# Kernel tuning notes

Measured on AMD Instinct MI355X. Metric: run time of the kernel, lower is better.

## Reference

```python
import jax, jax.numpy as jnp
import numpy as np
import math

B, S, D = 2, 2048, 1024
LKV, LQ = 512, 768
H, HD = 16, 64          # decop_rot_dim must equal head_dim (code reshapes rot proj to head_dim)
E, NS, K = 8, 2, 2      # routed experts, shared experts, top-k
EPS = 1e-6


def rmsnorm(x, w):
    xf = x.astype(jnp.float32)
    n = xf * jax.lax.rsqrt(jnp.mean(xf * xf, axis=-1, keepdims=True) + EPS)
    return w * n.astype(x.dtype)


def rope(x, cos, sin):
    # x: (B,S,H,HD); cos/sin: (S, HD//2). Pairs are consecutive elements (view_as_complex).
    xr = x.reshape(*x.shape[:-1], HD // 2, 2)
    x0, x1 = xr[..., 0], xr[..., 1]
    c = cos[None, :, None, :]
    s = sin[None, :, None, :]
    o0 = x0 * c - x1 * s
    o1 = x0 * s + x1 * c
    return jnp.stack([o0, o1], axis=-1).reshape(x.shape)


def _expert(x, W1, b1, W2, b2):
    # Expert: Linear -> ReLU -> Linear -> Dropout(0.5); dropout is identity at eval.
    return jax.nn.relu(x @ W1 + b1) @ W2 + b2


def setup_inputs() -> dict:
    key = jax.random.key(0)
    ks = jax.random.split(key, 20)
    g = lambda i, shape: jax.random.normal(ks[i], shape, jnp.float32) * 0.02
    inv_freq = 1.0 / (10000.0 ** (jnp.arange(0, HD, 2, dtype=jnp.float32) / HD))
    ang = jnp.arange(S, dtype=jnp.float32)[:, None] * inv_freq[None, :]  # (S, HD//2)
    return {
        'x': jax.random.normal(ks[0], (B, S, D), jnp.float32),
        'freqs_cos': jnp.cos(ang),
        'freqs_sin': jnp.sin(ang),
        'router_noise': jax.random.normal(ks[1], (B, S, E), jnp.float32),
        'rms1_w': jnp.ones((D,), jnp.float32),
        'rms2_w': jnp.ones((D,), jnp.float32),
        'w_lq': g(2, (D, LQ)), 'w_lkv': g(3, (D, LKV)),
        'w_q': g(4, (LQ, H * HD)), 'w_k': g(5, (LKV, H * HD)), 'w_v': g(6, (LKV, H * HD)),
        'w_qr': g(7, (LQ, H * HD)), 'b_qr': jnp.zeros((H * HD,), jnp.float32),
        'w_kr': g(8, (D, H * HD)), 'b_kr': jnp.zeros((H * HD,), jnp.float32),
        'w_o': g(9, (H * HD, D)), 'b_o': jnp.zeros((D,), jnp.float32),
        'w_route': g(10, (D, E)), 'b_route': jnp.zeros((E,), jnp.float32),
        'w_noise': g(11, (D, E)), 'b_noise': jnp.zeros((E,), jnp.float32),
        'rW1': g(12, (E, D, 4 * D)), 'rb1': jnp.zeros((E, 4 * D), jnp.float32),
        'rW2': g(13, (E, 4 * D, D)), 'rb2': jnp.zeros((E, D), jnp.float32),
        'sW1': g(14, (NS, D, 4 * D)), 'sb1': jnp.zeros((NS, 4 * D), jnp.float32),
        'sW2': g(15, (NS, 4 * D, D)), 'sb2': jnp.zeros((NS, D), jnp.float32),
    }


def _forward(x, freqs_cos, freqs_sin, router_noise, rms1_w, rms2_w,
             w_lq, w_lkv, w_q, w_k, w_v, w_qr, b_qr, w_kr, b_kr, w_o, b_o,
             w_route, b_route, w_noise, b_noise,
             rW1, rb1, rW2, rb2, sW1, sb1, sW2, sb2):
    Bq, Sq, Dq = x.shape
    # --- MLA attention branch ---
    h = rmsnorm(x, rms1_w)
    cq = h @ w_lq          # (B,S,LQ)
    ckv = h @ w_lkv        # (B,S,LKV)
    q = (cq @ w_q).reshape(Bq, Sq, H, HD)
    qr = rope((cq @ w_qr + b_qr).reshape(Bq, Sq, H, HD), freqs_cos, freqs_sin)
    k = (ckv @ w_k).reshape(Bq, Sq, H, HD)
    kr = rope((h @ w_kr + b_kr).reshape(Bq, Sq, H, HD), freqs_cos, freqs_sin)
    v = (ckv @ w_v).reshape(Bq, Sq, H, HD)
    qf = jnp.concatenate([q, qr], axis=-1)  # (B,S,H,2*HD)
    kf = jnp.concatenate([k, kr], axis=-1)
    scores = jnp.einsum('bqhd,bkhd->bhqk', qf, kf) / math.sqrt(HD)  # scale by sqrt(head_dim), as in source
    att = jax.nn.softmax(scores.astype(jnp.float32), axis=-1).astype(qf.dtype)
    attn_out = jnp.einsum('bhqk,bkhd->bqhd', att, v).reshape(Bq, Sq, H * HD)
    x = x + attn_out @ w_o + b_o
    # --- DeepSeek MoE branch ---
    h2 = rmsnorm(x, rms2_w)
    r_act = h2 @ w_route + b_route
    noisy = r_act + router_noise * jax.nn.softplus(h2 @ w_noise + b_noise)
    topv, idx = jax.lax.top_k(noisy, K)
    # softmax over -inf-filled sparse logits == softmax over top-k values scattered to idx
    wk = jax.nn.softmax(topv, axis=-1)  # (B,S,K)
    gate = jnp.einsum('btk,btke->bte', wk, jax.nn.one_hot(idx, E, dtype=h2.dtype))  # zeros off top-k
    f = jnp.zeros_like(h2)
    for i in range(E):  # fixed small expert loop; gate is exactly 0 for unrouted tokens
        f = f + gate[..., i:i + 1] * _expert(h2, rW1[i], rb1[i], rW2[i], rb2[i])
    for j in range(NS):
        f = f + _expert(h2, sW1[j], sb1[j], sW2[j], sb2[j])
    # DeepSeekMoE returns x_in + f_out where x_in = rmsnorm output; Block adds residual
    return x + h2 + f


def reference(x, freqs_cos, freqs_sin, router_noise, rms1_w, rms2_w,
              w_lq, w_lkv, w_q, w_k, w_v, w_qr, b_qr, w_kr, b_kr, w_o, b_o,
              w_route, b_route, w_noise, b_noise,
              rW1, rb1, rW2, rb2, sW1, sb1, sW2, sb2):
    return _forward(x, freqs_cos, freqs_sin, router_noise, rms1_w, rms2_w,
                    w_lq, w_lkv, w_q, w_k, w_v, w_qr, b_qr, w_kr, b_kr, w_o, b_o,
                    w_route, b_route, w_noise, b_noise,
                    rW1, rb1, rW2, rb2, sW1, sb1, sW2, sb2)
```

## Files before the change

### kernel.cpp

```cpp
#include <hip/hip_runtime.h>
#include <cstdint>

typedef unsigned short u16;
typedef unsigned int   u32;
typedef unsigned long long u64;
using short8 = __attribute__((ext_vector_type(8))) short;
using f32x4  = __attribute__((ext_vector_type(4))) float;

#define S_   2048
#define D_   1024
#define NTOK 4096

__device__ __forceinline__ u16 f2bf(float f){
  u32 u = __float_as_uint(f);
  u32 r = u + 0x7fffu + ((u >> 16) & 1u);
  return (u16)(r >> 16);
}
__device__ __forceinline__ float bf2f(u16 h){
  return __uint_as_float(((u32)h) << 16);
}
__device__ __forceinline__ void gld16(const void* g, void* l){
  __builtin_amdgcn_global_load_lds((__attribute__((address_space(1))) void*)(void*)g,
                                   (__attribute__((address_space(3))) void*)l, 16, 0, 0);
}

enum { F_OUTBF16=1, F_BIAS=2, F_RELU=4, F_RESID=8, F_GATEACC=16,
       F_GATHER=64, F_SCATTER=128, F_EXPB=512, F_SPLITK2=1024 };

template<int FLAGS>
__global__ void __launch_bounds__(256, 4)
gemm_k(const u16* __restrict__ A, int lda, long sAz,
       const u16* __restrict__ Bt, int ldb, long sBz,
       void* __restrict__ out, int ldo, long sOz,
       float* __restrict__ out2,
       const float* __restrict__ bias,
       const float* __restrict__ resid,
       const float* __restrict__ gv,
       const int* __restrict__ idx,
       const int* __restrict__ slotb,
       const int* __restrict__ cntp, int ebase,
       int K, int ncols)
{
  constexpr int BM = 128, BK = 32;
  const int tid = threadIdx.x;
  const int w = tid >> 6, l = tid & 63;
  const int wr = w >> 1, wc = w & 1;

  const int gx = gridDim.x, gy = gridDim.y;
  const int nwg = gx*gy*gridDim.z;
  const int flat = (blockIdx.z*gy + blockIdx.y)*gx + blockIdx.x;
  const int q8 = nwg >> 3, r8 = nwg & 7, xcd = flat & 7, off8 = flat >> 3;
  const int swz = (xcd < r8) ? (xcd*(q8+1) + off8)
                             : (r8*(q8+1) + (xcd-r8)*q8 + off8);
  const int tn = swz % gx;
  const int rest = swz / gx;
  const int tm = rest % gy;
  const int z  = rest / gy;
  const int ncol0 = tn * 128;

  int kh = 0, ze = z;
  if constexpr (FLAGS & F_SPLITK2){ kh = z & 1; ze = z >> 1; }

  int cnt = 0x7fffffff; long ofs = 0;
  if constexpr (FLAGS & (F_GATHER|F_SCATTER)){
    const int e = ebase + ze;
    cnt = cntp[e]; ofs = (long)cntp[8+e];
    if (tm*BM >= cnt) return;
  }

  const u16 *Abase, *Btbase;
  if constexpr (FLAGS & F_GATHER){
    Abase  = A;
    Btbase = Bt + (long)ze*sBz + (long)ncol0*ldb;
  } else if constexpr (FLAGS & F_SCATTER){
    Abase  = A + ofs*lda + (long)tm*BM*lda + (long)kh*K;
    Btbase = Bt + (long)ze*sBz + (long)ncol0*ldb + (long)kh*K;
  } else {
    Abase  = A  + (long)ze*sAz + (long)tm*BM*lda + (long)kh*K;
    Btbase = Bt + (long)ze*sBz + (long)ncol0*ldb + (long)kh*K;
  }

  const int r0 = tid >> 2, seg = tid & 3;
  long aoff0, aoff1;
  if constexpr (FLAGS & F_GATHER){
    const int p0 = tm*BM + r0, p1 = p0 + 64;
    const int t0 = (p0 < cnt) ? idx[ofs + p0] : 0;
    const int t1 = (p1 < cnt) ? idx[ofs + p1] : 0;
    aoff0 = (long)t0*lda; aoff1 = (long)t1*lda;
  } else {
    aoff0 = (long)r0*lda; aoff1 = (long)(r0+64)*lda;
  }
  const u16* pA0 = Abase + aoff0 + seg*8;
  const u16* pA1 = Abase + aoff1 + seg*8;
  const u16* pB0 = Btbase + (long)r0*ldb + seg*8;
  const u16* pB1 = Btbase + (long)(r0+64)*ldb + seg*8;

  __shared__ __align__(16) u16 As[2][BM*BK];
  __shared__ __align__(16) u16 Bs[2][BM*BK];

  f32x4 zero = {0.f,0.f,0.f,0.f};
  f32x4 acc[4][4];
  #pragma unroll
  for (int i=0;i<4;i++)
    #pragma unroll
    for (int j=0;j<4;j++) acc[i][j] = zero;

  const int NK = K >> 5;

  auto stage = [&](int buf, int kt){
    const int k0 = kt*BK;
    gld16(pA0 + k0, &As[buf][(w*64)*8]);
    gld16(pA1 + k0, &As[buf][(256 + w*64)*8]);
    gld16(pB0 + k0, &Bs[buf][(w*64)*8]);
    gld16(pB1 + k0, &Bs[buf][(256 + w*64)*8]);
  };

  stage(0,0);
  __syncthreads();

  for (int kt=0; kt<NK; ++kt){
    const int cur = kt & 1, nxt = cur ^ 1;
    if (kt+1 < NK) stage(nxt, kt+1);
    short8 a[4], b[4];
    #pragma unroll
    for (int m=0;m<4;m++){
      const int arow = wr*64 + m*16 + (l & 15);
      a[m] = *(const short8*)&As[cur][arow*BK + (l>>4)*8];
    }
    #pragma unroll
    for (int n=0;n<4;n++){
      const int brow = wc*64 + n*16 + (l & 15);
      b[n] = *(const short8*)&Bs[cur][brow*BK + (l>>4)*8];
    }
    #pragma unroll
    for (int m=0;m<4;m++)
      #pragma unroll
      for (int n=0;n<4;n++)
        acc[m][n] = __builtin_amdgcn_mfma_f32_16x16x32_bf16(a[m], b[n], acc[m][n], 0, 0, 0);
    __syncthreads();
  }

  float* outf = (float*)out + (long)z*sOz;
  u16*   outh = (u16*)out + (long)z*sOz;
  const float* bp = bias;
  if constexpr (FLAGS & F_EXPB) bp += (long)(ebase+ze)*ncols;
  const long row0 = (long)tm*BM + wr*64;
  #pragma unroll
  for (int m=0;m<4;m++){
    #pragma unroll
    for (int n=0;n<4;n++){
      const int col = ncol0 + wc*64 + n*16 + (l & 15);
      if (col < ncols){
        #pragma unroll
        for (int r=0;r<4;r++){
          const long row = row0 + m*16 + ((l>>4)*4) + r;
          float v = acc[m][n][r];
          if constexpr (FLAGS & F_BIAS){
            bool addb = true;
            if constexpr (FLAGS & F_SPLITK2) addb = (kh == 0);
            if (addb) v += bp[col];
          }
          if constexpr (FLAGS & F_RELU) v = fmaxf(v, 0.f);
          if constexpr (FLAGS & F_SCATTER){
            if (row < cnt){
              const long gs = ofs + row;
              const int tok = idx[gs];
              float* dst = (float*)out + (long)(slotb[gs]*2 + kh)*sOz;
              dst[(long)tok*ldo + col] = gv[gs] * v;
            }
          } else if constexpr (FLAGS & F_GATHER){
            if (row < cnt) outh[(ofs + row)*(long)ldo + col] = f2bf(v);
          } else if constexpr (FLAGS & F_GATEACC){
            outf[row*(long)ldo + col] += v;
          } else if constexpr (FLAGS & F_RESID){
            const long off = row*(long)ldo + col;
            outf[off] = resid[off] + v;
          } else if constexpr (FLAGS & F_OUTBF16){
            outh[row*(long)ldo + col] = f2bf(v);
          } else {
            outf[row*(long)ldo + col] = v;
          }
        }
      }
    }
  }
}

#define LDP 136

__global__ void __launch_bounds__(256, 2)
flash_k(const u16* __restrict__ qf, const u16* __restrict__ kf,
        const u16* __restrict__ vt, u16* __restrict__ attn)
{
  const int bh = blockIdx.x;
  const int qt = blockIdx.y;
  const int b = bh >> 4, h = bh & 15;
  const int tid = threadIdx.x, w = tid >> 6, l = tid & 63;
  const int l4 = l & 15, lh = l >> 4;

  const u16* Qb = qf + (long)b*4194304 + h*128;
  const u16* Kb = kf + (long)b*4194304 + h*128;
  const u16* Vb = vt + (long)bh*131072;
  u16* Ob = attn + (long)b*2097152 + h*64;

  short8 qa[2][4];
  #pragma unroll
  for (int m=0;m<2;m++)
    #pragma unroll
    for (int ks=0;ks<4;ks++){
      const long row = qt*128 + w*32 + m*16 + l4;
      qa[m][ks] = *(const short8*)(Qb + row*2048 + ks*32 + lh*8);
    }

  __shared__ __align__(16) u16 KPs[128*LDP];
  __shared__ __align__(16) u16 Vs[64*LDP];

  const float SCL = 0.125f * 1.44269504f;
  float mst[2][4], lst[2][4];
  f32x4 o_acc[2][4];
  #pragma unroll
  for (int m=0;m<2;m++)
    #pragma unroll
    for (int r=0;r<4;r++){ mst[m][r] = -3.0e38f; lst[m][r] = 0.f; }
  #pragma unroll
  for (int m=0;m<2;m++)
    #pragma unroll
    for (int n=0;n<4;n++) o_acc[m][n] = (f32x4){0.f,0.f,0.f,0.f};

  for (int t=0;t<16;t++){
    #pragma unroll
    for (int i=0;i<8;i++){
      const int c = i*256 + tid;
      const int kr = c >> 4, kc = (c & 15) * 8;
      const uint4 v = *(const uint4*)(Kb + (long)(t*128+kr)*2048 + kc);
      *(uint4*)&KPs[kr*LDP + kc] = v;
    }
    #pragma unroll
    for (int i=0;i<4;i++){
      const int c = i*256 + tid;
      const int vr = c >> 4, vc = (c & 15) * 8;
      const uint4 v = *(const uint4*)(Vb + (long)vr*2048 + t*128 + vc);
      *(uint4*)&Vs[vr*LDP + vc] = v;
    }
    __syncthreads();

    f32x4 s[2][8];
    #pragma unroll
    for (int m=0;m<2;m++)
      #pragma unroll
      for (int n=0;n<8;n++) s[m][n] = (f32x4){0.f,0.f,0.f,0.f};
    #pragma unroll
    for (int ks=0;ks<4;ks++){
      short8 bn[8];
      #pragma unroll
      for (int n=0;n<8;n++)
        bn[n] = *(const short8*)&KPs[(n*16+l4)*LDP + ks*32 + lh*8];
      #pragma unroll
      for (int m=0;m<2;m++)
        #pragma unroll
        for (int n=0;n<8;n++)
          s[m][n] = __builtin_amdgcn_mfma_f32_16x16x32_bf16(qa[m][ks], bn[n], s[m][n], 0,0,0);
    }
    __syncthreads();

    #pragma unroll
    for (int m=0;m<2;m++){
      #pragma unroll
      for (int r=0;r<4;r++){
        float pm = s[m][0][r];
        #pragma unroll
        for (int n=1;n<8;n++) pm = fmaxf(pm, s[m][n][r]);
        #pragma unroll
        for (int o=1;o<16;o<<=1) pm = fmaxf(pm, __shfl_xor(pm, o));
        const float mnew = fmaxf(mst[m][r], pm);
        const float sf = exp2f((mst[m][r] - mnew)*SCL);
        float rsum = 0.f;
        #pragma unroll
        for (int n=0;n<8;n++){
          const float p = exp2f((s[m][n][r] - mnew)*SCL);
          s[m][n][r] = p;
          rsum += p;
        }
        #pragma unroll
        for (int o=1;o<16;o<<=1) rsum += __shfl_xor(rsum, o);
        lst[m][r] = lst[m][r]*sf + rsum;
        mst[m][r] = mnew;
        #pragma unroll
        for (int n=0;n<4;n++) o_acc[m][n][r] *= sf;
      }
    }
    #pragma unroll
    for (int m=0;m<2;m++)
      #pragma unroll
      for (int n=0;n<8;n++)
        #pragma unroll
        for (int r=0;r<4;r++)
          KPs[(w*32 + m*16 + lh*4 + r)*LDP + n*16 + l4] = f2bf(s[m][n][r]);
    __syncthreads();

    #pragma unroll
    for (int ks=0;ks<4;ks++){
      short8 pa[2], vb[4];
      #pragma unroll
      for (int m=0;m<2;m++)
        pa[m] = *(const short8*)&KPs[(w*32 + m*16 + l4)*LDP + ks*32 + lh*8];
      #pragma unroll
      for (int n=0;n<4;n++)
        vb[n] = *(const short8*)&Vs[(n*16+l4)*LDP + ks*32 + lh*8];
      #pragma unroll
      for (int m=0;m<2;m++)
        #pragma unroll
        for (int n=0;n<4;n++)
          o_acc[m][n] = __builtin_amdgcn_mfma_f32_16x16x32_bf16(pa[m], vb[n], o_acc[m][n], 0,0,0);
    }
    __syncthreads();
  }

  #pragma unroll
  for (int m=0;m<2;m++){
    #pragma unroll
    for (int r=0;r<4;r++){
      const long row = qt*128 + w*32 + m*16 + lh*4 + r;
      const float inv = 1.f / lst[m][r];
      #pragma unroll
      for (int n=0;n<4;n++)
        Ob[row*1024 + n*16 + l4] = f2bf(o_acc[m][n][r] * inv);
    }
  }
}

__global__ void tpose_k(const float* __restrict__ src, u16* __restrict__ dst,
                        int K, int N, long szS, long szD)
{
  __shared__ u16 tile[32][36];
  const int t = threadIdx.x;
  src += (long)blockIdx.z*szS; dst += (long)blockIdx.z*szD;
  const int n0 = blockIdx.x*32, k0 = blockIdx.y*32;
  const int lr = t >> 3, lc = (t & 7) * 4;
  const float4 v = *(const float4*)&src[(long)(k0+lr)*N + n0 + lc];
  ushort4 tv; tv.x=f2bf(v.x); tv.y=f2bf(v.y); tv.z=f2bf(v.z); tv.w=f2bf(v.w);
  *(ushort4*)&tile[lr][lc] = tv;
  __syncthreads();
  ushort4 o;
  o.x = tile[lc+0][lr]; o.y = tile[lc+1][lr];
  o.z = tile[lc+2][lr]; o.w = tile[lc+3][lr];
  *(ushort4*)&dst[(long)(n0+lr)*K + k0 + lc] = o;
}

__global__ void vt_k(const u16* __restrict__ src, u16* __restrict__ dst)
{
  __shared__ u16 tile[32][36];
  const int t = threadIdx.x;
  const int z = blockIdx.z;
  const int b = z >> 4, h = z & 15;
  const int s0 = blockIdx.x*32, d0 = blockIdx.y*32;
  const int lr = t >> 3, lc = (t & 7) * 4;
  ushort4 v = *(const ushort4*)&src[(long)(b*2048 + s0+lr)*1024 + h*64 + d0 + lc];
  *(ushort4*)&tile[lr][lc] = v;
  __syncthreads();
  ushort4 o;
  o.x = tile[lc+0][lr]; o.y = tile[lc+1][lr];
  o.z = tile[lc+2][lr]; o.w = tile[lc+3][lr];
  *(ushort4*)&dst[(long)z*131072 + (long)(d0+lr)*2048 + s0 + lc] = o;
}

template<bool WF32>
__global__ void rmsnorm_k(const float* __restrict__ x, const float* __restrict__ w,
                          u16* __restrict__ ob, float* __restrict__ of)
{
  const int row = blockIdx.x, t = threadIdx.x;
  const float4 v = ((const float4*)(x + (long)row*D_))[t];
  float ss = v.x*v.x + v.y*v.y + v.z*v.z + v.w*v.w;
  #pragma unroll
  for (int o=32;o>0;o>>=1) ss += __shfl_down(ss, o);
  __shared__ float red[4];
  if ((t&63)==0) red[t>>6] = ss;
  __syncthreads();
  const float scale = rsqrtf((red[0]+red[1]+red[2]+red[3])*(1.0f/D_) + 1e-6f);
  const float4 wv = ((const float4*)w)[t];
  const float o0=v.x*scale*wv.x, o1=v.y*scale*wv.y, o2=v.z*scale*wv.z, o3=v.w*scale*wv.w;
  const long base = (long)row*D_ + t*4;
  uint2 p; p.x = (u32)f2bf(o0) | ((u32)f2bf(o1)<<16);
  p.y = (u32)f2bf(o2) | ((u32)f2bf(o3)<<16);
  *(uint2*)&ob[base] = p;
  if constexpr (WF32) *(float4*)&of[base] = make_float4(o0,o1,o2,o3);
}

__global__ void rope_concat_k(const u16* __restrict__ qt, const u16* __restrict__ qrt,
                              const u16* __restrict__ kt, const u16* __restrict__ krt,
                              const float* __restrict__ fc, const float* __restrict__ fs,
                              u16* __restrict__ qf, u16* __restrict__ kf)
{
  const int idx = blockIdx.x*256 + threadIdx.x;
  const int j = idx & 31, h = (idx>>5) & 15, bs = idx >> 9;
  if (bs >= NTOK) return;
  const int s = bs & (S_-1);
  const float c = fc[s*32+j], sn = fs[s*32+j];
  const long ib = (long)bs*1024 + h*64 + 2*j;
  const long ob = (long)bs*2048 + h*128 + 2*j;
  *(u32*)&qf[ob] = *(const u32*)&qt[ib];
  *(u32*)&kf[ob] = *(const u32*)&kt[ib];
  float x0 = bf2f(qrt[ib]), x1 = bf2f(qrt[ib+1]);
  *(u32*)&qf[ob+64] = (u32)f2bf(x0*c - x1*sn) | ((u32)f2bf(x0*sn + x1*c) << 16);
  x0 = bf2f(krt[ib]); x1 = bf2f(krt[ib+1]);
  *(u32*)&kf[ob+64] = (u32)f2bf(x0*c - x1*sn) | ((u32)f2bf(x0*sn + x1*c) << 16);
}

__global__ void topk_k(const float* __restrict__ h2, const float* __restrict__ wr,
                       const float* __restrict__ br, const float* __restrict__ wn,
                       const float* __restrict__ bn, const float* __restrict__ noise,
                       int* __restrict__ eids, float2* __restrict__ gates)
{
  const int tok = blockIdx.x, t = threadIdx.x;
  const float4 xv = ((const float4*)(h2 + (long)tok*D_))[t];
  const float xs[4] = {xv.x, xv.y, xv.z, xv.w};
  float ar[8], an[8];
  #pragma unroll
  for (int e=0;e<8;e++){ ar[e]=0.f; an[e]=0.f; }
  #pragma unroll
  for (int i=0;i<4;i++){
    const int d = t*4+i;
    const float* wrr = wr + d*8;
    const float* wnr = wn + d*8;
    #pragma unroll
    for (int e=0;e<8;e++){ ar[e] += xs[i]*wrr[e]; an[e] += xs[i]*wnr[e]; }
  }
  #pragma unroll
  for (int e=0;e<8;e++){
    #pragma unroll
    for (int o=32;o>0;o>>=1){ ar[e] += __shfl_down(ar[e], o); an[e] += __shfl_down(an[e], o); }
  }
  __shared__ float rr[4][8], rn[4][8];
  if ((t&63)==0){
    const int w4 = t>>6;
    #pragma unroll
    for (int e=0;e<8;e++){ rr[w4][e]=ar[e]; rn[w4][e]=an[e]; }
  }
  __syncthreads();
  if (t==0){
    float nz[8];
    #pragma unroll
    for (int e=0;e<8;e++){
      const float r  = rr[0][e]+rr[1][e]+rr[2][e]+rr[3][e] + br[e];
      const float ns = rn[0][e]+rn[1][e]+rn[2][e]+rn[3][e] + bn[e];
      const float sp = (ns > 20.f) ? ns : log1pf(expf(ns));
      nz[e] = r + noise[(long)tok*8+e]*sp;
    }
    int i0 = 0;
    #pragma unroll
    for (int e=1;e<8;e++) if (nz[e] > nz[i0]) i0 = e;
    int i1 = -1; float best = -3.0e38f;
    #pragma unroll
    for (int e=0;e<8;e++) if (e != i0 && nz[e] > best){ best = nz[e]; i1 = e; }
    const float e1  = expf(nz[i1]-nz[i0]);
    const float inv = 1.f/(1.f+e1);
    eids[tok] = i0 | (i1 << 8);
    gates[tok] = make_float2(inv, e1*inv);
  }
}

__global__ void __launch_bounds__(64)
hist_k(const int* __restrict__ eids, int* __restrict__ segcnt)
{
  const int b = blockIdx.x, t = threadIdx.x;
  const int id = eids[b*64 + t];
  const int i0 = id & 255, i1 = (id >> 8) & 255;
  #pragma unroll
  for (int e=0;e<8;e++){
    const u64 m0 = __ballot(i0==e);
    const u64 m1 = __ballot(i1==e);
    if (t==0) segcnt[e*64+b] = __popcll(m0) + __popcll(m1);
  }
}

__global__ void __launch_bounds__(64)
scan_k(const int* __restrict__ segcnt, int* __restrict__ segoff,
       int* __restrict__ cntoff)
{
  const int t = threadIdx.x;
  int base = 0;
  for (int e=0;e<8;e++){
    const int c = segcnt[e*64+t];
    int sc = c;
    #pragma unroll
    for (int o=1;o<64;o<<=1){ int u = __shfl_up(sc, o); if (t >= o) sc += u; }
    const int tot = __shfl(sc, 63);
    segoff[e*64+t] = base + (sc - c);
    if (t==0){ cntoff[e] = tot; cntoff[8+e] = base; }
    base += tot;
  }
}

__global__ void __launch_bounds__(64)
fill_k(const int* __restrict__ eids, const float2* __restrict__ gates,
       const int* __restrict__ segoff, int* __restrict__ idxb,
       float* __restrict__ gvb, int* __restrict__ slotb)
{
  const int b = blockIdx.x, t = threadIdx.x;
  const int tok = b*64 + t;
  const int id = eids[tok];
  const int i0 = id & 255, i1 = (id >> 8) & 255;
  const float2 g = gates[tok];
  const u64 below = ((u64)1 << t) - 1;
  #pragma unroll
  for (int e=0;e<8;e++){
    const u64 m0 = __ballot(i0==e);
    const u64 m1 = __ballot(i1==e);
    if (i0==e){
      const int pos = segoff[e*64+b] + __popcll(m0 & below);
      idxb[pos] = tok; gvb[pos] = g.x; slotb[pos] = 0;
    } else if (i1==e){
      const int pos = segoff[e*64+b] + __popcll(m0) + __popcll(m1 & below);
      idxb[pos] = tok; gvb[pos] = g.y; slotb[pos] = 1;
    }
  }
}

__global__ void addstore_k(const float* __restrict__ a, const float* __restrict__ b,
                           float* __restrict__ o, long n4)
{
  long i = (long)blockIdx.x*blockDim.x + threadIdx.x;
  const long stride = (long)gridDim.x*blockDim.x;
  for (; i<n4; i+=stride){
    const float4 va = ((const float4*)a)[i];
    const float4 vb = ((const float4*)b)[i];
    ((float4*)o)[i] = make_float4(va.x+vb.x, va.y+vb.y, va.z+vb.z, va.w+vb.w);
  }
}
__global__ void addacc4_k(const float* __restrict__ f0, const float* __restrict__ f1,
                          const float* __restrict__ f2, const float* __restrict__ f3,
                          float* __restrict__ o, long n4)
{
  long i = (long)blockIdx.x*blockDim.x + threadIdx.x;
  const long stride = (long)gridDim.x*blockDim.x;
  for (; i<n4; i+=stride){
    const float4 a = ((const float4*)f0)[i];
    const float4 b = ((const float4*)f1)[i];
    const float4 c = ((const float4*)f2)[i];
    const float4 d = ((const float4*)f3)[i];
    float4 vo = ((const float4*)o)[i];
    ((float4*)o)[i] = make_float4(vo.x+a.x+b.x+c.x+d.x, vo.y+a.y+b.y+c.y+d.y,
                                  vo.z+a.z+b.z+c.z+d.z, vo.w+a.w+b.w+c.w+d.w);
  }
}

extern "C" void kernel_launch(void* const* d_in, const int* in_sizes, int n_in,
                              void* d_out, int out_size, void* d_ws, size_t ws_size,
                              hipStream_t stream)
{
  const float* x      = (const float*)d_in[0];
  const float* fcos   = (const float*)d_in[1];
  const float* fsin   = (const float*)d_in[2];
  const float* rnoise = (const float*)d_in[3];
  const float* rms1w  = (const float*)d_in[4];
  const float* rms2w  = (const float*)d_in[5];
  const float* w_lq   = (const float*)d_in[6];
  const float* w_lkv  = (const float*)d_in[7];
  const float* w_q    = (const float*)d_in[8];
  const float* w_k    = (const float*)d_in[9];
  const float* w_v    = (const float*)d_in[10];
  const float* w_qr   = (const float*)d_in[11];
  const float* b_qr   = (const float*)d_in[12];
  const float* w_kr   = (const float*)d_in[13];
  const float* b_kr   = (const float*)d_in[14];
  const float* w_o    = (const float*)d_in[15];
  const float* b_o    = (const float*)d_in[16];
  const float* w_route= (const float*)d_in[17];
  const float* b_route= (const float*)d_in[18];
  const float* w_noise= (const float*)d_in[19];
  const float* b_noise= (const float*)d_in[20];
  const float* rW1    = (const float*)d_in[21];
  const float* rb1    = (const float*)d_in[22];
  const float* rW2    = (const float*)d_in[23];
  const float* rb2    = (const float*)d_in[24];
  const float* sW1    = (const float*)d_in[25];
  const float* sb1    = (const float*)d_in[26];
  const float* sW2    = (const float*)d_in[27];
  const float* sb2    = (const float*)d_in[28];

  if (ws_size < 195166208ULL) return;

  char* ws = (char*)d_ws;
  u16*   h_bf    = (u16*)(ws + 0);
  u16*   cq_bf   = (u16*)(ws + 8388608);
  u16*   ckv_bf  = (u16*)(ws + 14680064);
  u16*   v_bf    = (u16*)(ws + 18874368);
  u16*   qf      = (u16*)(ws + 27262976);
  u16*   kf      = (u16*)(ws + 44040192);
  u16*   vt      = (u16*)(ws + 60817408);
  u16*   attn_bf = (u16*)(ws + 69468160);
  float* x1      = (float*)(ws + 77856768);
  float* h2f     = (float*)(ws + 94633984);
  u16*   h2_bf   = (u16*)(ws + 111411200);
  float* fb      = (float*)(ws + 119799808);
  u16*   Wt_g    = (u16*)(ws + 77856768);
  int*   cntoff  = (int*)(ws + 189005824);
  int*   eids    = (int*)(ws + 189006080);
  float2* gatesb = (float2*)(ws + 189022464);
  int*   idxb    = (int*)(ws + 189055232);
  float* gvb     = (float*)(ws + 189088000);
  int*   slotb   = (int*)(ws + 189120768);
  u16*   wo_t    = (u16*)(ws + 189153536);
  int*   segcnt  = (int*)(ws + 191250560);
  int*   segoff  = (int*)(ws + 191252608);
  u16*   q_tmp   = (u16*)(ws + 77856768);
  u16*   qr_tmp  = (u16*)(ws + 86245376);
  u16*   k_tmp   = (u16*)(ws + 94633984);
  u16*   kr_tmp  = (u16*)(ws + 103022592);
  u16*   inter   = (u16*)(ws + 0);
  u16*   wlq_t   = (u16*)(ws + 119799808);
  u16*   wlkv_t  = (u16*)(ws + 121372672);
  u16*   wq_t    = (u16*)(ws + 122421248);
  u16*   wqr_t   = (u16*)(ws + 123994112);
  u16*   wk_t    = (u16*)(ws + 125566976);
  u16*   wkr_t   = (u16*)(ws + 126615552);
  u16*   wv_t    = (u16*)(ws + 128712704);

  const dim3 blk(256,1,1);
  #define GEMM(FL, GRID, ...) gemm_k<FL><<<GRID, blk, 0, stream>>>(__VA_ARGS__)
  #define NOSPARSE nullptr,nullptr,nullptr,nullptr,nullptr,nullptr,nullptr,0

  tpose_k<<<dim3(24,32),blk,0,stream>>>(w_lq,  wlq_t, 1024, 768, 0,0);
  tpose_k<<<dim3(16,32),blk,0,stream>>>(w_lkv, wlkv_t,1024, 512, 0,0);
  tpose_k<<<dim3(32,24),blk,0,stream>>>(w_q,   wq_t,   768,1024, 0,0);
  tpose_k<<<dim3(32,24),blk,0,stream>>>(w_qr,  wqr_t,  768,1024, 0,0);
  tpose_k<<<dim3(32,16),blk,0,stream>>>(w_k,   wk_t,   512,1024, 0,0);
  tpose_k<<<dim3(32,32),blk,0,stream>>>(w_kr,  wkr_t, 1024,1024, 0,0);
  tpose_k<<<dim3(32,16),blk,0,stream>>>(w_v,   wv_t,   512,1024, 0,0);
  tpose_k<<<dim3(32,32),blk,0,stream>>>(w_o,   wo_t,  1024,1024, 0,0);

  rmsnorm_k<false><<<NTOK, blk, 0, stream>>>(x, rms1w, h_bf, nullptr);

  GEMM(F_OUTBF16, dim3(6,32,1),  h_bf,1024,0,  wlq_t,1024,0,  cq_bf,768,0,  NOSPARSE, 1024, 768);
  GEMM(F_OUTBF16, dim3(4,32,1),  h_bf,1024,0,  wlkv_t,1024,0, ckv_bf,512,0, NOSPARSE, 1024, 512);
  GEMM(F_OUTBF16, dim3(8,32,1),  cq_bf,768,0,  wq_t,768,0,    q_tmp,1024,0, NOSPARSE, 768, 1024);
  GEMM(F_OUTBF16|F_BIAS, dim3(8,32,1), cq_bf,768,0, wqr_t,768,0, qr_tmp,1024,0,
       nullptr, b_qr, nullptr,nullptr,nullptr,nullptr,nullptr,0, 768, 1024);
  GEMM(F_OUTBF16, dim3(8,32,1),  ckv_bf,512,0, wk_t,512,0,    k_tmp,1024,0, NOSPARSE, 512, 1024);
  GEMM(F_OUTBF16|F_BIAS, dim3(8,32,1), h_bf,1024,0, wkr_t,1024,0, kr_tmp,1024,0,
       nullptr, b_kr, nullptr,nullptr,nullptr,nullptr,nullptr,0, 1024, 1024);
  GEMM(F_OUTBF16, dim3(8,32,1),  ckv_bf,512,0, wv_t,512,0,    v_bf,1024,0,  NOSPARSE, 512, 1024);

  rope_concat_k<<<8192, blk, 0, stream>>>(q_tmp, qr_tmp, k_tmp, kr_tmp, fcos, fsin, qf, kf);
  vt_k<<<dim3(64,2,32), blk, 0, stream>>>(v_bf, vt);

  flash_k<<<dim3(32,16), blk, 0, stream>>>(qf, kf, vt, attn_bf);

  GEMM(F_BIAS|F_RESID, dim3(8,32,1), attn_bf,1024,0, wo_t,1024,0, x1,1024,0,
       nullptr, b_o, x, nullptr,nullptr,nullptr,nullptr,0, 1024, 1024);
  rmsnorm_k<true><<<NTOK, blk, 0, stream>>>(x1, rms2w, h2_bf, h2f);
  topk_k<<<NTOK, blk, 0, stream>>>(h2f, w_route, b_route, w_noise, b_noise, rnoise,
                                   eids, gatesb);
  hist_k<<<64, 64, 0, stream>>>(eids, segcnt);
  scan_k<<<1, 64, 0, stream>>>(segcnt, segoff, cntoff);
  fill_k<<<64, 64, 0, stream>>>(eids, gatesb, segoff, idxb, gvb, slotb);
  addstore_k<<<2048, blk, 0, stream>>>(x1, h2f, (float*)d_out, 1048576L);
  hipMemsetAsync(fb, 0, 67108864, stream);

  for (int g=0; g<2; ++g){
    const int eb = g*4;
    tpose_k<<<dim3(128,32,4),blk,0,stream>>>(rW1 + (long)eb*4194304, Wt_g, 1024, 4096,
                                             4194304L, 4194304L);
    GEMM(F_OUTBF16|F_BIAS|F_RELU|F_GATHER|F_EXPB, dim3(32,32,4),
         h2_bf,1024,0, Wt_g,1024,4194304L, inter,4096,0,
         nullptr, rb1, nullptr, nullptr, idxb, nullptr, cntoff, eb, 1024, 4096);
    tpose_k<<<dim3(32,128,4),blk,0,stream>>>(rW2 + (long)eb*4194304, Wt_g, 4096, 1024,
                                             4194304L, 4194304L);
    GEMM(F_BIAS|F_SCATTER|F_EXPB|F_SPLITK2, dim3(8,32,8),
         inter,4096,0, Wt_g,4096,4194304L, fb,1024,4194304L,
         nullptr, rb2, nullptr, gvb, idxb, slotb, cntoff, eb, 2048, 1024);
  }

  for (int j=0;j<2;j++){
    tpose_k<<<dim3(128,32,1),blk,0,stream>>>(sW1 + (long)j*4194304, Wt_g, 1024, 4096, 0,0);
    GEMM(F_OUTBF16|F_BIAS|F_RELU, dim3(32,32,1), h2_bf,1024,0, Wt_g,1024,0, inter,4096,0,
         nullptr, sb1 + j*4096, nullptr,nullptr,nullptr,nullptr,nullptr,0, 1024, 4096);
    tpose_k<<<dim3(32,128,1),blk,0,stream>>>(sW2 + (long)j*4194304, Wt_g, 4096, 1024, 0,0);
    GEMM(F_BIAS|F_GATEACC|F_SPLITK2, dim3(8,32,2),
         inter,4096,0, Wt_g,4096,0, fb + (long)j*2*4194304L,1024,4194304L,
         nullptr, sb2 + j*1024, nullptr,nullptr,nullptr,nullptr,nullptr,0, 2048, 1024);
  }

  addacc4_k<<<2048, blk, 0, stream>>>(fb, fb+4194304L, fb+8388608L, fb+12582912L,
                                      (float*)d_out, 1048576L);
}
```

Measured before the change: 1.178 ms.

## Merge Q/QR, K/V projections and shared-expert GEMMs into wider launches

```diff
diff --git a/kernel.cpp b/kernel.cpp
--- a/kernel.cpp
+++ b/kernel.cpp
@@ -25,10 +25,10 @@
 }
 
 enum { F_OUTBF16=1, F_BIAS=2, F_RELU=4, F_RESID=8, F_GATEACC=16,
-       F_GATHER=64, F_SCATTER=128, F_EXPB=512, F_SPLITK2=1024 };
+       F_GATHER=64, F_SCATTER=128, F_EXPB=512, F_SPLITK2=1024, F_BIASHI=2048 };
 
 template<int FLAGS>
-__global__ void __launch_bounds__(256, 4)
+__global__ void __launch_bounds__(256, 5)
 gemm_k(const u16* __restrict__ A, int lda, long sAz,
        const u16* __restrict__ Bt, int ldb, long sBz,
        void* __restrict__ out, int ldo, long sOz,
@@ -159,6 +159,9 @@
             bool addb = true;
             if constexpr (FLAGS & F_SPLITK2) addb = (kh == 0);
             if (addb) v += bp[col];
+          }
+          if constexpr (FLAGS & F_BIASHI){
+            if (col >= 1024) v += bias[col - 1024];
           }
           if constexpr (FLAGS & F_RELU) v = fmaxf(v, 0.f);
           if constexpr (FLAGS & F_SCATTER){
@@ -347,7 +350,7 @@
   *(ushort4*)&dst[(long)(n0+lr)*K + k0 + lc] = o;
 }
 
-__global__ void vt_k(const u16* __restrict__ src, u16* __restrict__ dst)
+__global__ void vt_k(const u16* __restrict__ kv, u16* __restrict__ dst)
 {
   __shared__ u16 tile[32][36];
   const int t = threadIdx.x;
@@ -355,7 +358,7 @@
   const int b = z >> 4, h = z & 15;
   const int s0 = blockIdx.x*32, d0 = blockIdx.y*32;
   const int lr = t >> 3, lc = (t & 7) * 4;
-  ushort4 v = *(const ushort4*)&src[(long)(b*2048 + s0+lr)*1024 + h*64 + d0 + lc];
+  ushort4 v = *(const ushort4*)&kv[(long)(b*2048 + s0+lr)*2048 + 1024 + h*64 + d0 + lc];
   *(ushort4*)&tile[lr][lc] = v;
   __syncthreads();
   ushort4 o;
@@ -386,8 +389,8 @@
   if constexpr (WF32) *(float4*)&of[base] = make_float4(o0,o1,o2,o3);
 }
 
-__global__ void rope_concat_k(const u16* __restrict__ qt, const u16* __restrict__ qrt,
-                              const u16* __restrict__ kt, const u16* __restrict__ krt,
+__global__ void rope_concat_k(const u16* __restrict__ qqr, const u16* __restrict__ kv,
+                              const u16* __restrict__ krt,
                               const float* __restrict__ fc, const float* __restrict__ fs,
                               u16* __restrict__ qf, u16* __restrict__ kf)
 {
@@ -396,13 +399,14 @@
   if (bs >= NTOK) return;
   const int s = bs & (S_-1);
   const float c = fc[s*32+j], sn = fs[s*32+j];
-  const long ib = (long)bs*1024 + h*64 + 2*j;
+  const long ib2 = (long)bs*2048 + h*64 + 2*j;
+  const long ib1 = (long)bs*1024 + h*64 + 2*j;
   const long ob = (long)bs*2048 + h*128 + 2*j;
-  *(u32*)&qf[ob] = *(const u32*)&qt[ib];
-  *(u32*)&kf[ob] = *(const u32*)&kt[ib];
-  float x0 = bf2f(qrt[ib]), x1 = bf2f(qrt[ib+1]);
+  *(u32*)&qf[ob] = *(const u32*)&qqr[ib2];
+  *(u32*)&kf[ob] = *(const u32*)&kv[ib2];
+  float x0 = bf2f(qqr[ib2+1024]), x1 = bf2f(qqr[ib2+1025]);
   *(u32*)&qf[ob+64] = (u32)f2bf(x0*c - x1*sn) | ((u32)f2bf(x0*sn + x1*c) << 16);
-  x0 = bf2f(krt[ib]); x1 = bf2f(krt[ib+1]);
+  x0 = bf2f(krt[ib1]); x1 = bf2f(krt[ib1+1]);
   *(u32*)&kf[ob+64] = (u32)f2bf(x0*c - x1*sn) | ((u32)f2bf(x0*sn + x1*c) << 16);
 }
 
@@ -584,7 +588,7 @@
   u16*   h_bf    = (u16*)(ws + 0);
   u16*   cq_bf   = (u16*)(ws + 8388608);
   u16*   ckv_bf  = (u16*)(ws + 14680064);
-  u16*   v_bf    = (u16*)(ws + 18874368);
+  u16*   kr_tmp  = (u16*)(ws + 18874368);
   u16*   qf      = (u16*)(ws + 27262976);
   u16*   kf      = (u16*)(ws + 44040192);
   u16*   vt      = (u16*)(ws + 60817408);
@@ -603,18 +607,14 @@
   u16*   wo_t    = (u16*)(ws + 189153536);
   int*   segcnt  = (int*)(ws + 191250560);
   int*   segoff  = (int*)(ws + 191252608);
-  u16*   q_tmp   = (u16*)(ws + 77856768);
-  u16*   qr_tmp  = (u16*)(ws + 86245376);
-  u16*   k_tmp   = (u16*)(ws + 94633984);
-  u16*   kr_tmp  = (u16*)(ws + 103022592);
+  u16*   qqr     = (u16*)(ws + 77856768);
+  u16*   kv      = (u16*)(ws + 94633984);
   u16*   inter   = (u16*)(ws + 0);
   u16*   wlq_t   = (u16*)(ws + 119799808);
-  u16*   wlkv_t  = (u16*)(ws + 121372672);
-  u16*   wq_t    = (u16*)(ws + 122421248);
-  u16*   wqr_t   = (u16*)(ws + 123994112);
-  u16*   wk_t    = (u16*)(ws + 125566976);
-  u16*   wkr_t   = (u16*)(ws + 126615552);
-  u16*   wv_t    = (u16*)(ws + 128712704);
+  u16*   wlkv_t  = (u16*)(ws + 121899008);
+  u16*   wqqr_t  = (u16*)(ws + 123996160);
+  u16*   wkv_t   = (u16*)(ws + 127141888);
+  u16*   wkr_t   = (u16*)(ws + 129239040);
 
   const dim3 blk(256,1,1);
   #define GEMM(FL, GRID, ...) gemm_k<FL><<<GRID, blk, 0, stream>>>(__VA_ARGS__)
@@ -622,27 +622,25 @@
 
   tpose_k<<<dim3(24,32),blk,0,stream>>>(w_lq,  wlq_t, 1024, 768, 0,0);
   tpose_k<<<dim3(16,32),blk,0,stream>>>(w_lkv, wlkv_t,1024, 512, 0,0);
-  tpose_k<<<dim3(32,24),blk,0,stream>>>(w_q,   wq_t,   768,1024, 0,0);
-  tpose_k<<<dim3(32,24),blk,0,stream>>>(w_qr,  wqr_t,  768,1024, 0,0);
-  tpose_k<<<dim3(32,16),blk,0,stream>>>(w_k,   wk_t,   512,1024, 0,0);
+  tpose_k<<<dim3(32,24),blk,0,stream>>>(w_q,   wqqr_t,            768,1024, 0,0);
+  tpose_k<<<dim3(32,24),blk,0,stream>>>(w_qr,  wqqr_t + 1024*768, 768,1024, 0,0);
+  tpose_k<<<dim3(32,16),blk,0,stream>>>(w_k,   wkv_t,             512,1024, 0,0);
+  tpose_k<<<dim3(32,16),blk,0,stream>>>(w_v,   wkv_t + 1024*512,  512,1024, 0,0);
   tpose_k<<<dim3(32,32),blk,0,stream>>>(w_kr,  wkr_t, 1024,1024, 0,0);
-  tpose_k<<<dim3(32,16),blk,0,stream>>>(w_v,   wv_t,   512,1024, 0,0);
   tpose_k<<<dim3(32,32),blk,0,stream>>>(w_o,   wo_t,  1024,1024, 0,0);
 
   rmsnorm_k<false><<<NTOK, blk, 0, stream>>>(x, rms1w, h_bf, nullptr);
 
   GEMM(F_OUTBF16, dim3(6,32,1),  h_bf,1024,0,  wlq_t,1024,0,  cq_bf,768,0,  NOSPARSE, 1024, 768);
   GEMM(F_OUTBF16, dim3(4,32,1),  h_bf,1024,0,  wlkv_t,1024,0, ckv_bf,512,0, NOSPARSE, 1024, 512);
-  GEMM(F_OUTBF16, dim3(8,32,1),  cq_bf,768,0,  wq_t,768,0,    q_tmp,1024,0, NOSPARSE, 768, 1024);
-  GEMM(F_OUTBF16|F_BIAS, dim3(8,32,1), cq_bf,768,0, wqr_t,768,0, qr_tmp,1024,0,
-       nullptr, b_qr, nullptr,nullptr,nullptr,nullptr,nullptr,0, 768, 1024);
-  GEMM(F_OUTBF16, dim3(8,32,1),  ckv_bf,512,0, wk_t,512,0,    k_tmp,1024,0, NOSPARSE, 512, 1024);
+  GEMM(F_OUTBF16|F_BIASHI, dim3(16,32,1), cq_bf,768,0,  wqqr_t,768,0, qqr,2048,0,
+       nullptr, b_qr, nullptr,nullptr,nullptr,nullptr,nullptr,0, 768, 2048);
+  GEMM(F_OUTBF16, dim3(16,32,1), ckv_bf,512,0, wkv_t,512,0,  kv,2048,0,  NOSPARSE, 512, 2048);
   GEMM(F_OUTBF16|F_BIAS, dim3(8,32,1), h_bf,1024,0, wkr_t,1024,0, kr_tmp,1024,0,
        nullptr, b_kr, nullptr,nullptr,nullptr,nullptr,nullptr,0, 1024, 1024);
-  GEMM(F_OUTBF16, dim3(8,32,1),  ckv_bf,512,0, wv_t,512,0,    v_bf,1024,0,  NOSPARSE, 512, 1024);
-
-  rope_concat_k<<<8192, blk, 0, stream>>>(q_tmp, qr_tmp, k_tmp, kr_tmp, fcos, fsin, qf, kf);
-  vt_k<<<dim3(64,2,32), blk, 0, stream>>>(v_bf, vt);
+
+  rope_concat_k<<<8192, blk, 0, stream>>>(qqr, kv, kr_tmp, fcos, fsin, qf, kf);
+  vt_k<<<dim3(64,2,32), blk, 0, stream>>>(kv, vt);
 
   flash_k<<<dim3(32,16), blk, 0, stream>>>(qf, kf, vt, attn_bf);
 
@@ -671,15 +669,13 @@
          nullptr, rb2, nullptr, gvb, idxb, slotb, cntoff, eb, 2048, 1024);
   }
 
-  for (int j=0;j<2;j++){
-    tpose_k<<<dim3(128,32,1),blk,0,stream>>>(sW1 + (long)j*4194304, Wt_g, 1024, 4096, 0,0);
-    GEMM(F_OUTBF16|F_BIAS|F_RELU, dim3(32,32,1), h2_bf,1024,0, Wt_g,1024,0, inter,4096,0,
-         nullptr, sb1 + j*4096, nullptr,nullptr,nullptr,nullptr,nullptr,0, 1024, 4096);
-    tpose_k<<<dim3(32,128,1),blk,0,stream>>>(sW2 + (long)j*4194304, Wt_g, 4096, 1024, 0,0);
-    GEMM(F_BIAS|F_GATEACC|F_SPLITK2, dim3(8,32,2),
-         inter,4096,0, Wt_g,4096,0, fb + (long)j*2*4194304L,1024,4194304L,
-         nullptr, sb2 + j*1024, nullptr,nullptr,nullptr,nullptr,nullptr,0, 2048, 1024);
-  }
+  tpose_k<<<dim3(128,32,2),blk,0,stream>>>(sW1, Wt_g, 1024, 4096, 4194304L, 4194304L);
+  GEMM(F_OUTBF16|F_BIAS|F_RELU, dim3(64,32,1), h2_bf,1024,0, Wt_g,1024,0, inter,8192,0,
+       nullptr, sb1, nullptr,nullptr,nullptr,nullptr,nullptr,0, 1024, 8192);
+  tpose_k<<<dim3(32,128,2),blk,0,stream>>>(sW2, Wt_g, 4096, 1024, 4194304L, 4194304L);
+  GEMM(F_BIAS|F_GATEACC|F_EXPB|F_SPLITK2, dim3(8,32,4),
+       inter,8192,4096, Wt_g,4096,4194304L, fb,1024,4194304L,
+       nullptr, sb2, nullptr,nullptr,nullptr,nullptr,nullptr,0, 2048, 1024);
 
   addacc4_k<<<2048, blk, 0, stream>>>(fb, fb+4194304L, fb+8388608L, fb+12582912L,
                                       (float*)d_out, 1048576L);
```

After: 1.757 ms. +49.1%, slower.
